# Kernel tuning notes

Measured on AMD Instinct MI355X. Metric: run time of the kernel, lower is better.

Reference implementation:

```python
import jax, jax.numpy as jnp
import numpy as np

# sym2 (== db2) decomposition filters from pywt
_DEC_LO = np.array([-0.12940952255126037, 0.22414386804185735,
                    0.8365163037378079, 0.48296291314453416], dtype=np.float32)
_DEC_HI = np.array([-0.48296291314453416, 0.8365163037378079,
                    -0.22414386804185735, -0.12940952255126037], dtype=np.float32)
# pytorch_wavelets flips the filters before torch's cross-correlation conv
H0R = jnp.asarray(_DEC_LO[::-1].copy())
H1R = jnp.asarray(_DEC_HI[::-1].copy())
L = 4  # filter length
LEVEL = 3


def afb1d(x):
    """One level of DWT (mode='zero'), x: (B, C, N) -> (lo, hi) each (B, C, (N+L-1)//2)."""
    N = x.shape[-1]
    out = (N + L - 1) // 2              # pywt dwt_coeff_len for mode='zero'
    p = 2 * (out - 1) - N + L           # total pad
    if p % 2 == 1:                      # odd-length signals get one extra zero at the end
        x = jnp.pad(x, ((0, 0), (0, 0), (0, 1)))
    ph = p // 2
    x = jnp.pad(x, ((0, 0), (0, 0), (ph, ph)))
    # strided windows: y[n] = sum_k h[k] * x_pad[2n + k]
    wins = [x[..., k:k + 2 * out:2][..., :out] for k in range(L)]
    lo = sum(H0R[k] * wins[k] for k in range(L))
    hi = sum(H1R[k] * wins[k] for k in range(L))
    return lo, hi


def wavelet_packet(x, level=LEVEL):
    # breadth-first, lo-first ordering == lexicographic sort of 'a'/'d' paths
    bands = [x]
    for _ in range(level):
        nxt = []
        for b in bands:
            lo, hi = afb1d(b)
            nxt.append(lo)
            nxt.append(hi)
        bands = nxt
    return bands


def setup_inputs() -> dict:
    key = jax.random.key(0)
    k1, k2, k3 = jax.random.split(key, 3)
    B, C, N, num_classes = 131072, 3, 50, 5
    total_features = 192  # 8 leaves * 3 channels * 8 samples
    x = jax.random.normal(k1, (B, C, N), dtype=jnp.float32)
    W = jax.random.normal(k2, (num_classes, total_features), dtype=jnp.float32) * 0.05
    b = jax.random.normal(k3, (num_classes,), dtype=jnp.float32) * 0.05
    return {"x": x, "W": W, "b": b}


def reference(x, W, b):
    bands = wavelet_packet(x)
    B = x.shape[0]
    feats = jnp.concatenate([band.reshape(B, -1) for band in bands], axis=1)  # (B, 192)
    return feats @ W.T + b                          # (B, 5)
```

## Files before the change

kernel.cpp:

```cpp
#include <hip/hip_runtime.h>

struct Amat { float a[64][50]; };

constexpr Amat makeA() {
    constexpr float h0[4] = { 0.48296291314453416f,  0.8365163037378079f,
                              0.22414386804185735f, -0.12940952255126037f};
    constexpr float h1[4] = {-0.12940952255126037f, -0.22414386804185735f,
                              0.8365163037378079f,  -0.48296291314453416f};
    float L1[2][26][50] = {};
    for (int band = 0; band < 2; ++band)
        for (int m = 0; m < 26; ++m)
            for (int n = 0; n < 50; ++n) {
                int k = n - 2 * m + 2;
                L1[band][m][n] = (k >= 0 && k < 4) ? (band ? h1[k] : h0[k]) : 0.0f;
            }
    float L2[4][14][50] = {};
    for (int j = 0; j < 4; ++j)
        for (int m = 0; m < 14; ++m)
            for (int n = 0; n < 50; ++n) {
                float acc = 0.0f;
                for (int k = 0; k < 4; ++k) {
                    int p = 2 * m + k - 2;
                    if (p >= 0 && p < 26)
                        acc += (j & 1 ? h1[k] : h0[k]) * L1[j >> 1][p][n];
                }
                L2[j][m][n] = acc;
            }
    Amat A = {};
    for (int j = 0; j < 8; ++j)
        for (int m = 0; m < 8; ++m)
            for (int n = 0; n < 50; ++n) {
                float acc = 0.0f;
                for (int k = 0; k < 4; ++k) {
                    int p = 2 * m + k - 2;
                    if (p >= 0 && p < 14)
                        acc += (j & 1 ? h1[k] : h0[k]) * L2[j >> 1][p][n];
                }
                A.a[j * 8 + m][n] = acc;
            }
    return A;
}

__device__ __constant__ Amat cA = makeA();

__global__ __launch_bounds__(256) void build_M(const float* __restrict__ W,
                                               const float* __restrict__ bias,
                                               float* __restrict__ Mg) {
    __shared__ float sW[960];
    const int tid = threadIdx.x;
    #pragma unroll
    for (int t = 0; t < 4; ++t) {
        const int idx = tid + t * 256;
        if (idx < 960) sW[idx] = W[idx];
    }
    __syncthreads();

    if (tid < 150) {
        const int c = tid / 50, n = tid - c * 50;
        float m0 = 0.f, m1 = 0.f, m2 = 0.f, m3 = 0.f, m4 = 0.f;
        #pragma unroll 16
        for (int f = 0; f < 64; ++f) {
            const float av = cA.a[f][n];
            const int wj = (f >> 3) * 24 + c * 8 + (f & 7);
            m0 = fmaf(sW[0 * 192 + wj], av, m0);
            m1 = fmaf(sW[1 * 192 + wj], av, m1);
            m2 = fmaf(sW[2 * 192 + wj], av, m2);
            m3 = fmaf(sW[3 * 192 + wj], av, m3);
            m4 = fmaf(sW[4 * 192 + wj], av, m4);
        }
        Mg[0 * 160 + tid] = m0;
        Mg[1 * 160 + tid] = m1;
        Mg[2 * 160 + tid] = m2;
        Mg[3 * 160 + tid] = m3;
        Mg[4 * 160 + tid] = m4;
    } else if (tid < 160) {
        #pragma unroll
        for (int k = 0; k < 5; ++k) Mg[k * 160 + tid] = 0.f;
    } else if (tid < 165) {
        Mg[800 + (tid - 160)] = bias[tid - 160];
    }
}

#define RPB2 32

__global__ __launch_bounds__(256) void dwt_gemv(const float* __restrict__ x,
                                                const float* __restrict__ Mg,
                                                float* __restrict__ out) {
    __shared__ float sM[805];
    __shared__ float sO[RPB2 * 5];
    const int tid = threadIdx.x;
    #pragma unroll
    for (int t = 0; t < 4; ++t) {
        const int idx = tid + t * 256;
        if (idx < 805) sM[idx] = Mg[idx];
    }
    __syncthreads();

    const int g  = tid >> 4;
    const int lg = tid & 15;
    const size_t rA = (size_t)blockIdx.x * RPB2 + g;
    const size_t rB = rA + 16;
    const float2* __restrict__ xa = (const float2*)(x + rA * 150);
    const float2* __restrict__ xb = (const float2*)(x + rB * 150);

    float a0 = 0.f, a1 = 0.f, a2 = 0.f, a3 = 0.f, a4 = 0.f;
    float b0 = 0.f, b1 = 0.f, b2 = 0.f, b3 = 0.f, b4 = 0.f;

    #pragma unroll
    for (int j = 0; j < 5; ++j) {
        const int fi = j * 16 + lg;
        if (fi < 75) {
            const float2 xva = xa[fi];
            const float2 xvb = xb[fi];
            const int d = 2 * fi;
            { const float2 m = *(const float2*)&sM[0 * 160 + d];
              a0 = fmaf(m.x, xva.x, a0); a0 = fmaf(m.y, xva.y, a0);
              b0 = fmaf(m.x, xvb.x, b0); b0 = fmaf(m.y, xvb.y, b0); }
            { const float2 m = *(const float2*)&sM[1 * 160 + d];
              a1 = fmaf(m.x, xva.x, a1); a1 = fmaf(m.y, xva.y, a1);
              b1 = fmaf(m.x, xvb.x, b1); b1 = fmaf(m.y, xvb.y, b1); }
            { const float2 m = *(const float2*)&sM[2 * 160 + d];
              a2 = fmaf(m.x, xva.x, a2); a2 = fmaf(m.y, xva.y, a2);
              b2 = fmaf(m.x, xvb.x, b2); b2 = fmaf(m.y, xvb.y, b2); }
            { const float2 m = *(const float2*)&sM[3 * 160 + d];
              a3 = fmaf(m.x, xva.x, a3); a3 = fmaf(m.y, xva.y, a3);
              b3 = fmaf(m.x, xvb.x, b3); b3 = fmaf(m.y, xvb.y, b3); }
            { const float2 m = *(const float2*)&sM[4 * 160 + d];
              a4 = fmaf(m.x, xva.x, a4); a4 = fmaf(m.y, xva.y, a4);
              b4 = fmaf(m.x, xvb.x, b4); b4 = fmaf(m.y, xvb.y, b4); }
        }
    }

    #pragma unroll
    for (int o = 1; o < 16; o <<= 1) {
        a0 += __shfl_xor(a0, o); a1 += __shfl_xor(a1, o);
        a2 += __shfl_xor(a2, o); a3 += __shfl_xor(a3, o);
        a4 += __shfl_xor(a4, o);
        b0 += __shfl_xor(b0, o); b1 += __shfl_xor(b1, o);
        b2 += __shfl_xor(b2, o); b3 += __shfl_xor(b3, o);
        b4 += __shfl_xor(b4, o);
    }

    if (lg == 0) {
        float* oa = &sO[g * 5];
        oa[0] = a0 + sM[800]; oa[1] = a1 + sM[801]; oa[2] = a2 + sM[802];
        oa[3] = a3 + sM[803]; oa[4] = a4 + sM[804];
        float* ob = &sO[(g + 16) * 5];
        ob[0] = b0 + sM[800]; ob[1] = b1 + sM[801]; ob[2] = b2 + sM[802];
        ob[3] = b3 + sM[803]; ob[4] = b4 + sM[804];
    }
    __syncthreads();

    if (tid < RPB2 * 5)
        out[(size_t)blockIdx.x * (RPB2 * 5) + tid] = sO[tid];
}

extern "C" void kernel_launch(void* const* d_in, const int* in_sizes, int n_in,
                              void* d_out, int out_size, void* d_ws, size_t ws_size,
                              hipStream_t stream) {
    const float* x    = (const float*)d_in[0];
    const float* W    = (const float*)d_in[1];
    const float* bias = (const float*)d_in[2];
    float*       out  = (float*)d_out;
    float*       Mg   = (float*)d_ws;

    build_M<<<1, 256, 0, stream>>>(W, bias, Mg);

    const int B    = in_sizes[0] / 150;
    const int grid = B / RPB2;
    dwt_gemv<<<grid, 256, 0, stream>>>(x, Mg, out);
}
```

Baseline: 28.83 us.

## Process four rows per thread group with interleaved M layout and DPP reductions

```diff
diff --git a/kernel.cpp b/kernel.cpp
--- a/kernel.cpp
+++ b/kernel.cpp
@@ -68,26 +68,33 @@
             m3 = fmaf(sW[3 * 192 + wj], av, m3);
             m4 = fmaf(sW[4 * 192 + wj], av, m4);
         }
-        Mg[0 * 160 + tid] = m0;
-        Mg[1 * 160 + tid] = m1;
-        Mg[2 * 160 + tid] = m2;
-        Mg[3 * 160 + tid] = m3;
-        Mg[4 * 160 + tid] = m4;
+        const int base = (tid >> 1) * 10 + (tid & 1);
+        Mg[base + 0] = m0;
+        Mg[base + 2] = m1;
+        Mg[base + 4] = m2;
+        Mg[base + 6] = m3;
+        Mg[base + 8] = m4;
     } else if (tid < 160) {
+        const int base = (tid >> 1) * 10 + (tid & 1);
         #pragma unroll
-        for (int k = 0; k < 5; ++k) Mg[k * 160 + tid] = 0.f;
+        for (int k = 0; k < 5; ++k) Mg[base + 2 * k] = 0.f;
     } else if (tid < 165) {
         Mg[800 + (tid - 160)] = bias[tid - 160];
     }
 }
 
-#define RPB2 32
+template <int N>
+__device__ __forceinline__ float ror_add(float v) {
+    const int r = __builtin_amdgcn_update_dpp(
+        __float_as_int(v), __float_as_int(v), 0x120 + N, 0xF, 0xF, false);
+    return v + __int_as_float(r);
+}
 
 __global__ __launch_bounds__(256) void dwt_gemv(const float* __restrict__ x,
                                                 const float* __restrict__ Mg,
                                                 float* __restrict__ out) {
     __shared__ float sM[805];
-    __shared__ float sO[RPB2 * 5];
+    __shared__ float sO[64 * 5];
     const int tid = threadIdx.x;
     #pragma unroll
     for (int t = 0; t < 4; ++t) {
@@ -98,61 +105,54 @@
 
     const int g  = tid >> 4;
     const int lg = tid & 15;
-    const size_t rA = (size_t)blockIdx.x * RPB2 + g;
-    const size_t rB = rA + 16;
-    const float2* __restrict__ xa = (const float2*)(x + rA * 150);
-    const float2* __restrict__ xb = (const float2*)(x + rB * 150);
+    const size_t r0 = (size_t)blockIdx.x * 64 + g;
+    const float2* __restrict__ xr = (const float2*)x;
 
-    float a0 = 0.f, a1 = 0.f, a2 = 0.f, a3 = 0.f, a4 = 0.f;
-    float b0 = 0.f, b1 = 0.f, b2 = 0.f, b3 = 0.f, b4 = 0.f;
+    float a0[5] = {0,0,0,0,0};
+    float a1[5] = {0,0,0,0,0};
+    float a2[5] = {0,0,0,0,0};
+    float a3[5] = {0,0,0,0,0};
 
     #pragma unroll
-    for (int j = 0; j < 5; ++j) {
-        const int fi = j * 16 + lg;
-        if (fi < 75) {
-            const float2 xva = xa[fi];
-            const float2 xvb = xb[fi];
-            const int d = 2 * fi;
-            { const float2 m = *(const float2*)&sM[0 * 160 + d];
-              a0 = fmaf(m.x, xva.x, a0); a0 = fmaf(m.y, xva.y, a0);
-              b0 = fmaf(m.x, xvb.x, b0); b0 = fmaf(m.y, xvb.y, b0); }
-            { const float2 m = *(const float2*)&sM[1 * 160 + d];
-              a1 = fmaf(m.x, xva.x, a1); a1 = fmaf(m.y, xva.y, a1);
-              b1 = fmaf(m.x, xvb.x, b1); b1 = fmaf(m.y, xvb.y, b1); }
-            { const float2 m = *(const float2*)&sM[2 * 160 + d];
-              a2 = fmaf(m.x, xva.x, a2); a2 = fmaf(m.y, xva.y, a2);
-              b2 = fmaf(m.x, xvb.x, b2); b2 = fmaf(m.y, xvb.y, b2); }
-            { const float2 m = *(const float2*)&sM[3 * 160 + d];
-              a3 = fmaf(m.x, xva.x, a3); a3 = fmaf(m.y, xva.y, a3);
-              b3 = fmaf(m.x, xvb.x, b3); b3 = fmaf(m.y, xvb.y, b3); }
-            { const float2 m = *(const float2*)&sM[4 * 160 + d];
-              a4 = fmaf(m.x, xva.x, a4); a4 = fmaf(m.y, xva.y, a4);
-              b4 = fmaf(m.x, xvb.x, b4); b4 = fmaf(m.y, xvb.y, b4); }
+    for (int s = 0; s < 5; ++s) {
+        const int fi  = s * 16 + lg;
+        const int fx  = (fi < 75) ? fi : 74;
+        const float2 v0 = xr[(r0     ) * 75 + fx];
+        const float2 v1 = xr[(r0 + 16) * 75 + fx];
+        const float2 v2 = xr[(r0 + 32) * 75 + fx];
+        const float2 v3 = xr[(r0 + 48) * 75 + fx];
+        #pragma unroll
+        for (int k = 0; k < 5; ++k) {
+            const float2 m = *(const float2*)&sM[fi * 10 + k * 2];
+            a0[k] = fmaf(m.y, v0.y, fmaf(m.x, v0.x, a0[k]));
+            a1[k] = fmaf(m.y, v1.y, fmaf(m.x, v1.x, a1[k]));
+            a2[k] = fmaf(m.y, v2.y, fmaf(m.x, v2.x, a2[k]));
+            a3[k] = fmaf(m.y, v3.y, fmaf(m.x, v3.x, a3[k]));
         }
     }
 
     #pragma unroll
-    for (int o = 1; o < 16; o <<= 1) {
-        a0 += __shfl_xor(a0, o); a1 += __shfl_xor(a1, o);
-        a2 += __shfl_xor(a2, o); a3 += __shfl_xor(a3, o);
-        a4 += __shfl_xor(a4, o);
-        b0 += __shfl_xor(b0, o); b1 += __shfl_xor(b1, o);
-        b2 += __shfl_xor(b2, o); b3 += __shfl_xor(b3, o);
-        b4 += __shfl_xor(b4, o);
+    for (int k = 0; k < 5; ++k) {
+        a0[k] = ror_add<1>(ror_add<2>(ror_add<4>(ror_add<8>(a0[k]))));
+        a1[k] = ror_add<1>(ror_add<2>(ror_add<4>(ror_add<8>(a1[k]))));
+        a2[k] = ror_add<1>(ror_add<2>(ror_add<4>(ror_add<8>(a2[k]))));
+        a3[k] = ror_add<1>(ror_add<2>(ror_add<4>(ror_add<8>(a3[k]))));
     }
 
     if (lg == 0) {
-        float* oa = &sO[g * 5];
-        oa[0] = a0 + sM[800]; oa[1] = a1 + sM[801]; oa[2] = a2 + sM[802];
-        oa[3] = a3 + sM[803]; oa[4] = a4 + sM[804];
-        float* ob = &sO[(g + 16) * 5];
-        ob[0] = b0 + sM[800]; ob[1] = b1 + sM[801]; ob[2] = b2 + sM[802];
-        ob[3] = b3 + sM[803]; ob[4] = b4 + sM[804];
+        #pragma unroll
+        for (int k = 0; k < 5; ++k) {
+            const float b = sM[800 + k];
+            sO[(g     ) * 5 + k] = a0[k] + b;
+            sO[(g + 16) * 5 + k] = a1[k] + b;
+            sO[(g + 32) * 5 + k] = a2[k] + b;
+            sO[(g + 48) * 5 + k] = a3[k] + b;
+        }
     }
     __syncthreads();
 
-    if (tid < RPB2 * 5)
-        out[(size_t)blockIdx.x * (RPB2 * 5) + tid] = sO[tid];
+    for (int idx = tid; idx < 320; idx += 256)
+        out[(size_t)blockIdx.x * 320 + idx] = sO[idx];
 }
 
 extern "C" void kernel_launch(void* const* d_in, const int* in_sizes, int n_in,
@@ -167,6 +167,6 @@
     build_M<<<1, 256, 0, stream>>>(W, bias, Mg);
 
     const int B    = in_sizes[0] / 150;
-    const int grid = B / RPB2;
+    const int grid = B / 64;
     dwt_gemv<<<grid, 256, 0, stream>>>(x, Mg, out);
 }
```

Result: faster. 26.52 us (-8.0%).
